# Optimization experiments

Measured on AMD Instinct MI355X. Metric: run time of the kernel, lower is better.

The kernel has to match this reference:

```python
import jax, jax.numpy as jnp
import numpy as np

C_IN = 128
C_INNER = 128


def setup_inputs() -> dict:
    key = jax.random.key(0)
    ks = jax.random.split(key, 9)
    b, c, h, w = 4, C_IN, 64, 64
    s = 1.0 / np.sqrt(c)
    x = jax.random.normal(ks[0], (b, c, h, w), dtype=jnp.float32)
    Wq = jax.random.normal(ks[1], (C_INNER, C_IN), dtype=jnp.float32) * s
    bq = jnp.zeros((C_INNER,), dtype=jnp.float32)
    Wk = jax.random.normal(ks[2], (C_INNER, C_IN), dtype=jnp.float32) * s
    bk = jnp.zeros((C_INNER,), dtype=jnp.float32)
    Wv = jax.random.normal(ks[3], (C_INNER, C_IN), dtype=jnp.float32) * s
    bv = jnp.zeros((C_INNER,), dtype=jnp.float32)
    Wo = jax.random.normal(ks[4], (C_IN, C_INNER), dtype=jnp.float32) * (1.0 / np.sqrt(C_INNER))
    bo = jnp.zeros((C_IN,), dtype=jnp.float32)
    return {"x": x, "Wq": Wq, "bq": bq, "Wk": Wk, "bk": bk,
            "Wv": Wv, "bv": bv, "Wo": Wo, "bo": bo}


def _conv1x1(x, W, bias):
    # x: (b,c,h,w), W: (o,c) -> (b,o,h,w)
    return jnp.einsum('oc,bchw->bohw', W, x) + bias[None, :, None, None]


def reference(x, Wq, bq, Wk, bk, Wv, bv, Wo, bo):
    b, c, h, w = x.shape
    ci = Wq.shape[0]
    n = h * w
    q = _conv1x1(x, Wq, bq).reshape(b, ci, n)          # (b, ci, n)
    k = _conv1x1(x, Wk, bk).reshape(b, ci, n)          # (b, ci, n)
    v = _conv1x1(x, Wv, bv).reshape(b, ci, n)          # (b, ci, n)
    # attn = softmax(q^T @ k) over keys
    attn = jnp.einsum('bci,bcj->bij', q, k)            # (b, n, n)
    attn = jax.nn.softmax(attn, axis=-1)
    out = jnp.einsum('bij,bcj->bci', attn, v)          # (b, ci, n)
    out = out.reshape(b, ci, h, w)
    out = _conv1x1(out, Wo, bo)
    return out + x
```

## Files before the change

### kernel.cpp

```cpp
#include <hip/hip_runtime.h>
#include <math.h>
#include <stdint.h>

#define CDIM 128
#define NTOT 4096

typedef _Float16 f16x8 __attribute__((ext_vector_type(8)));
typedef float floatx4 __attribute__((ext_vector_type(4)));

static __device__ __forceinline__ floatx4 mfma16(f16x8 a, f16x8 b, floatx4 c) {
    return __builtin_amdgcn_mfma_f32_16x16x32_f16(a, b, c, 0, 0, 0);
}
static __device__ __forceinline__ unsigned short f2h(float f) {
    _Float16 h = (_Float16)f;
    return __builtin_bit_cast(unsigned short, h);
}
static __device__ __forceinline__ float h2f(unsigned short u) {
    return (float)__builtin_bit_cast(_Float16, u);
}

#define SWZ(row, cc) ((((row) << 7)) + ((((cc) ^ ((row) & 15))) << 3))
#define SWZ8(row, cc) ((((row) << 6)) + ((((cc) ^ ((row) & 7))) << 3))

static __device__ __forceinline__ void gload_lds16(const void* g, void* l) {
    __builtin_amdgcn_global_load_lds(
        (const __attribute__((address_space(1))) void*)g,
        (__attribute__((address_space(3))) void*)l, 16, 0, 0);
}

__global__ __launch_bounds__(256) void wcvt_kernel(
    const float* __restrict__ Wq, const float* __restrict__ Wk,
    const float* __restrict__ Wv, const float* __restrict__ Wo,
    unsigned short* __restrict__ Wh)
{
    const float* src = (blockIdx.y == 0) ? Wq : (blockIdx.y == 1) ? Wk
                     : (blockIdx.y == 2) ? Wv : Wo;
    const int i = (blockIdx.x * 256 + threadIdx.x) * 4;
    float4 f = *(const float4*)&src[i];
    ushort4 u = { f2h(f.x), f2h(f.y), f2h(f.z), f2h(f.w) };
    *(ushort4*)&Wh[(size_t)blockIdx.y * 16384 + i] = u;
}

__global__ __launch_bounds__(256) void qkv_proj_kernel(
    const float* __restrict__ x, const unsigned short* __restrict__ Wh,
    const float* __restrict__ bq, const float* __restrict__ bk,
    const float* __restrict__ bv,
    unsigned short* __restrict__ qo, unsigned short* __restrict__ ko,
    unsigned short* __restrict__ vo)
{
    __shared__ __align__(16) unsigned short Xs[16][136];

    const int t = threadIdx.x;
    const int bid = blockIdx.x;
    const int swz = ((bid & 7) << 7) | (bid >> 3);
    const int b = swz >> 8;
    const int n0 = (swz & 255) * 16;
    const int w = t >> 6, quad = (t >> 4) & 3, l15 = t & 15;

    {
        const int n = (t & 3) * 4;
        const int c = (t >> 2) * 2;
        float4 xr[2];
        #pragma unroll
        for (int j = 0; j < 2; ++j)
            xr[j] = *(const float4*)&x[((size_t)b * CDIM + c + j) * NTOT + n0 + n];
        #pragma unroll
        for (int k = 0; k < 4; ++k) {
            ushort2 u;
            u.x = f2h(((const float*)&xr[0])[k]);
            u.y = f2h(((const float*)&xr[1])[k]);
            *(ushort2*)&Xs[n + k][c] = u;
        }
    }
    __syncthreads();

    f16x8 xf[4];
    #pragma unroll
    for (int f = 0; f < 4; ++f)
        xf[f] = *(const f16x8*)&Xs[l15][f * 32 + quad * 8];

    #pragma unroll
    for (int s = 0; s < 2; ++s) {
        const unsigned short* Wm = Wh + (size_t)s * 16384;
        const float* bias = s ? bk : bq;
        unsigned short* dst = s ? ko : qo;
        #pragma unroll
        for (int ot = 0; ot < 2; ++ot) {
            const int o = w * 32 + ot * 16;
            floatx4 acc = (floatx4){0.f, 0.f, 0.f, 0.f};
            #pragma unroll
            for (int f = 0; f < 4; ++f) {
                f16x8 aW = *(const f16x8*)
                    &Wm[(size_t)(o + l15) * CDIM + f * 32 + quad * 8];
                acc = mfma16(aW, xf[f], acc);
            }
            const int ob = o + quad * 4;
            ushort4 u;
            u.x = f2h(acc[0] + bias[ob + 0]);
            u.y = f2h(acc[1] + bias[ob + 1]);
            u.z = f2h(acc[2] + bias[ob + 2]);
            u.w = f2h(acc[3] + bias[ob + 3]);
            *(ushort4*)&dst[((size_t)b * NTOT + n0 + l15) * CDIM + ob] = u;
        }
    }
    {
        const unsigned short* Wm = Wh + 2 * 16384;
        #pragma unroll
        for (int ot = 0; ot < 2; ++ot) {
            const int o = w * 32 + ot * 16 + l15;
            floatx4 acc = (floatx4){0.f, 0.f, 0.f, 0.f};
            #pragma unroll
            for (int f = 0; f < 4; ++f) {
                f16x8 bW = *(const f16x8*)
                    &Wm[(size_t)o * CDIM + f * 32 + quad * 8];
                acc = mfma16(xf[f], bW, acc);
            }
            const float bv_ = bv[o];
            ushort4 u;
            u.x = f2h(acc[0] + bv_); u.y = f2h(acc[1] + bv_);
            u.z = f2h(acc[2] + bv_); u.w = f2h(acc[3] + bv_);
            *(ushort4*)&vo[((size_t)b * CDIM + o) * NTOT + n0 + quad * 4] = u;
        }
    }
}

__global__ __launch_bounds__(256, 2) void attn_kernel(
    const unsigned short* __restrict__ qg,
    const unsigned short* __restrict__ kg,
    const unsigned short* __restrict__ vg,
    unsigned short* __restrict__ Op,
    float* __restrict__ Ms, float* __restrict__ Ls)
{
    __shared__ __align__(16) unsigned short Kb[2][64 * 128];
    __shared__ __align__(16) unsigned short Vb[2][128 * 64];
    __shared__ __align__(16) unsigned short Ps[128 * 64];

    const int t = threadIdx.x;
    const int w = t >> 6, quad = (t >> 4) & 3, l15 = t & 15;

    const int bid = blockIdx.x;
    const int swz = ((bid & 7) << 6) | (bid >> 3);
    const int gidx = swz >> 5;
    const int b = gidx & 3;
    const int z = gidx >> 2;
    const int i0 = (swz & 31) * 128;
    const int jbase = z * 1024;
    const size_t vbase = (size_t)b * CDIM * NTOT;

    f16x8 bQ[2][4];
    #pragma unroll
    for (int nt = 0; nt < 2; ++nt) {
        const size_t qrow = ((size_t)b * NTOT + i0 + w * 32 + nt * 16 + l15) * CDIM;
        #pragma unroll
        for (int f = 0; f < 4; ++f)
            bQ[nt][f] = *(const f16x8*)&qg[qrow + f * 32 + quad * 8];
    }

    auto stage = [&](unsigned short* Kd, unsigned short* Vd, int j0) {
        const size_t kbase = ((size_t)b * NTOT + j0) * CDIM;
        const size_t vrow0 = vbase + j0;
        #pragma unroll
        for (int r = 0; r < 4; ++r) {
            const int flat = r * 256 + t;
            const int ldsoff = (r * 256 + (t & ~63)) * 8;
            const int krow = flat >> 4, kcc = flat & 15;
            gload_lds16(&kg[kbase + (size_t)krow * CDIM + ((kcc ^ (krow & 15)) << 3)],
                        &Kd[ldsoff]);
        }
        #pragma unroll
        for (int r = 0; r < 4; ++r) {
            const int flat = r * 256 + t;
            const int ldsoff = (r * 256 + (t & ~63)) * 8;
            const int vrow = flat >> 3, vcc = flat & 7;
            gload_lds16(&vg[vrow0 + (size_t)vrow * NTOT + ((vcc ^ (vrow & 7)) << 3)],
                        &Vd[ldsoff]);
        }
    };

    floatx4 accO[2][8];
    #pragma unroll
    for (int nt = 0; nt < 2; ++nt)
        #pragma unroll
        for (int dt = 0; dt < 8; ++dt) accO[nt][dt] = (floatx4){0.f, 0.f, 0.f, 0.f};
    float m_run[2] = {-INFINITY, -INFINITY};
    float l_part[2] = {0.f, 0.f};

    stage(Kb[0], Vb[0], jbase);

    for (int iter = 0; iter < 16; ++iter) {
        const int cur = iter & 1;

        asm volatile("s_waitcnt vmcnt(0) lgkmcnt(0)" ::: "memory");
        __builtin_amdgcn_s_barrier();

        if (iter < 15) stage(Kb[cur ^ 1], Vb[cur ^ 1], jbase + (iter + 1) * 64);

        floatx4 accT[2][4];
        #pragma unroll
        for (int nt = 0; nt < 2; ++nt)
            #pragma unroll
            for (int jt = 0; jt < 4; ++jt) accT[nt][jt] = (floatx4){0.f, 0.f, 0.f, 0.f};
        __builtin_amdgcn_s_setprio(1);
        #pragma unroll
        for (int jt = 0; jt < 4; ++jt)
            #pragma unroll
            for (int f = 0; f < 4; ++f) {
                f16x8 aK = *(const f16x8*)&Kb[cur][SWZ(jt * 16 + l15, f * 4 + quad)];
                accT[0][jt] = mfma16(aK, bQ[0][f], accT[0][jt]);
                accT[1][jt] = mfma16(aK, bQ[1][f], accT[1][jt]);
            }
        __builtin_amdgcn_s_setprio(0);

        ushort4 pu[2][4];
        #pragma unroll
        for (int nt = 0; nt < 2; ++nt) {
            float tm = accT[nt][0][0];
            #pragma unroll
            for (int jt = 0; jt < 4; ++jt)
                #pragma unroll
                for (int r = 0; r < 4; ++r) tm = fmaxf(tm, accT[nt][jt][r]);
            tm = fmaxf(tm, __shfl_xor(tm, 16));
            tm = fmaxf(tm, __shfl_xor(tm, 32));
            if (__ballot(tm > m_run[nt] + 8.f)) {
                const float m_new = fmaxf(m_run[nt], tm);
                const float alpha = __expf(m_run[nt] - m_new);
                m_run[nt] = m_new;
                l_part[nt] *= alpha;
                #pragma unroll
                for (int dt = 0; dt < 8; ++dt) {
                    accO[nt][dt][0] *= alpha; accO[nt][dt][1] *= alpha;
                    accO[nt][dt][2] *= alpha; accO[nt][dt][3] *= alpha;
                }
            }
            const float mcur = m_run[nt];
            float ps = 0.f;
            #pragma unroll
            for (int jt = 0; jt < 4; ++jt) {
                float p0 = __expf(accT[nt][jt][0] - mcur);
                float p1 = __expf(accT[nt][jt][1] - mcur);
                float p2 = __expf(accT[nt][jt][2] - mcur);
                float p3 = __expf(accT[nt][jt][3] - mcur);
                ps += (p0 + p1) + (p2 + p3);
                pu[nt][jt].x = f2h(p0); pu[nt][jt].y = f2h(p1);
                pu[nt][jt].z = f2h(p2); pu[nt][jt].w = f2h(p3);
            }
            l_part[nt] += ps;
        }

        #pragma unroll
        for (int nt = 0; nt < 2; ++nt) {
            const int prow = w * 32 + nt * 16 + l15;
            #pragma unroll
            for (int jt = 0; jt < 4; ++jt)
                *(ushort4*)&Ps[SWZ8(prow, 2 * jt + (quad >> 1)) + (quad & 1) * 4] =
                    pu[nt][jt];
        }
        asm volatile("s_waitcnt lgkmcnt(0)" ::: "memory");
        __builtin_amdgcn_sched_barrier(0);

        f16x8 bP[2][2];
        #pragma unroll
        for (int nt = 0; nt < 2; ++nt) {
            const int prow = w * 32 + nt * 16 + l15;
            #pragma unroll
            for (int kb = 0; kb < 2; ++kb)
                bP[nt][kb] = *(const f16x8*)&Ps[SWZ8(prow, kb * 4 + quad)];
        }
        __builtin_amdgcn_s_setprio(1);
        #pragma unroll
        for (int dt = 0; dt < 8; ++dt)
            #pragma unroll
            for (int kb = 0; kb < 2; ++kb) {
                f16x8 aV = *(const f16x8*)&Vb[cur][SWZ8(dt * 16 + l15, kb * 4 + quad)];
                accO[0][dt] = mfma16(aV, bP[0][kb], accO[0][dt]);
                accO[1][dt] = mfma16(aV, bP[1][kb], accO[1][dt]);
            }
        __builtin_amdgcn_s_setprio(0);
    }

    #pragma unroll
    for (int nt = 0; nt < 2; ++nt) {
        float lf = l_part[nt];
        lf += __shfl_xor(lf, 16);
        lf += __shfl_xor(lf, 32);
        const float inv = 1.0f / lf;
        const size_t orow =
            (((size_t)z * 4 + b) * NTOT + i0 + w * 32 + nt * 16 + l15) * CDIM;
        #pragma unroll
        for (int dt = 0; dt < 8; ++dt) {
            ushort4 u;
            u.x = f2h(accO[nt][dt][0] * inv); u.y = f2h(accO[nt][dt][1] * inv);
            u.z = f2h(accO[nt][dt][2] * inv); u.w = f2h(accO[nt][dt][3] * inv);
            *(ushort4*)&Op[orow + dt * 16 + quad * 4] = u;
        }
        if (quad == 0) {
            const int idx = (z * 4 + b) * NTOT + i0 + w * 32 + nt * 16 + l15;
            Ms[idx] = m_run[nt];
            Ls[idx] = lf;
        }
    }
}

__global__ __launch_bounds__(256) void out_proj_kernel(
    const unsigned short* __restrict__ Op,
    const float* __restrict__ Ms, const float* __restrict__ Ls,
    const unsigned short* __restrict__ Woh, const float* __restrict__ bo,
    const float* __restrict__ x, float* __restrict__ out)
{
    __shared__ __align__(16) unsigned short As[32][136];

    const int t = threadIdx.x, b = blockIdx.y, n0 = blockIdx.x * 32;
    const int zo = blockIdx.z * 64;
    const int w = t >> 6, quad = (t >> 4) & 3, l15 = t & 15;

    const size_t PER = (size_t)NTOT * 4 * CDIM;

    #pragma unroll
    for (int r = 0; r < 2; ++r) {
        int flat = r * 256 + t;
        int row = flat >> 4, c16 = (flat & 15) * 8;
        const int bn = b * NTOT + n0 + row;
        float m0 = Ms[bn], m1 = Ms[bn + 16384], m2 = Ms[bn + 32768], m3 = Ms[bn + 49152];
        float M = fmaxf(fmaxf(m0, m1), fmaxf(m2, m3));
        float w0 = Ls[bn]         * __expf(m0 - M);
        float w1 = Ls[bn + 16384] * __expf(m1 - M);
        float w2 = Ls[bn + 32768] * __expf(m2 - M);
        float w3 = Ls[bn + 49152] * __expf(m3 - M);
        const float inv = 1.0f / (w0 + w1 + w2 + w3);
        w0 *= inv; w1 *= inv; w2 *= inv; w3 *= inv;

        const size_t base = (size_t)bn * CDIM + c16;
        uint4 a0 = *(const uint4*)&Op[base];
        uint4 a1 = *(const uint4*)&Op[PER + base];
        uint4 a2 = *(const uint4*)&Op[2 * PER + base];
        uint4 a3 = *(const uint4*)&Op[3 * PER + base];
        const unsigned short* p0 = (const unsigned short*)&a0;
        const unsigned short* p1 = (const unsigned short*)&a1;
        const unsigned short* p2 = (const unsigned short*)&a2;
        const unsigned short* p3 = (const unsigned short*)&a3;
        unsigned short mv[8];
        #pragma unroll
        for (int j = 0; j < 8; ++j)
            mv[j] = f2h(w0 * h2f(p0[j]) + w1 * h2f(p1[j]) +
                        w2 * h2f(p2[j]) + w3 * h2f(p3[j]));
        *(uint4*)&As[row][c16] = *(const uint4*)mv;
    }
    __syncthreads();

    const int nt = w & 1, oh = w >> 1;
    f16x8 bA[4];
    #pragma unroll
    for (int f = 0; f < 4; ++f)
        bA[f] = *(const f16x8*)&As[nt * 16 + l15][f * 32 + quad * 8];

    #pragma unroll
    for (int ot = 0; ot < 2; ++ot) {
        const int o = zo + oh * 32 + ot * 16;
        floatx4 acc = (floatx4){0.f, 0.f, 0.f, 0.f};
        #pragma unroll
        for (int f = 0; f < 4; ++f) {
            f16x8 aW = *(const f16x8*)
                &Woh[(size_t)(o + l15) * CDIM + f * 32 + quad * 8];
            acc = mfma16(aW, bA[f], acc);
        }
        const int ob = o + quad * 4;
        #pragma unroll
        for (int r = 0; r < 4; ++r) {
            size_t idx = ((size_t)b * CDIM + ob + r) * NTOT + n0 + nt * 16 + l15;
            out[idx] = acc[r] + bo[ob + r] + x[idx];
        }
    }
}

extern "C" void kernel_launch(void* const* d_in, const int* in_sizes, int n_in,
                              void* d_out, int out_size, void* d_ws, size_t ws_size,
                              hipStream_t stream)
{
    const float* x  = (const float*)d_in[0];
    const float* Wq = (const float*)d_in[1];
    const float* bq = (const float*)d_in[2];
    const float* Wk = (const float*)d_in[3];
    const float* bk = (const float*)d_in[4];
    const float* Wv = (const float*)d_in[5];
    const float* bv = (const float*)d_in[6];
    const float* Wo = (const float*)d_in[7];
    const float* bo = (const float*)d_in[8];
    float* out = (float*)d_out;

    const size_t PER = (size_t)4 * CDIM * NTOT;
    unsigned short* q_ws  = (unsigned short*)d_ws;
    unsigned short* k_ws  = q_ws + PER;
    unsigned short* v_ws  = k_ws + PER;
    unsigned short* op_ws = v_ws + PER;
    float*          ms_ws = (float*)(op_ws + 4 * PER);
    float*          ls_ws = ms_ws + 4 * 16384;
    unsigned short* wh_ws = (unsigned short*)(ls_ws + 4 * 16384);

    wcvt_kernel<<<dim3(16, 4), dim3(256), 0, stream>>>(Wq, Wk, Wv, Wo, wh_ws);
    qkv_proj_kernel<<<dim3(1024), dim3(256), 0, stream>>>(
        x, wh_ws, bq, bk, bv, q_ws, k_ws, v_ws);
    attn_kernel<<<dim3(512), dim3(256), 0, stream>>>(
        q_ws, k_ws, v_ws, op_ws, ms_ws, ls_ws);
    out_proj_kernel<<<dim3(128, 4, 2), dim3(256), 0, stream>>>(
        op_ws, ms_ws, ls_ws, wh_ws + 3 * 16384, bo, x, out);
}
```

Before: 150.5 us.

## Shrink attention tiles to 64 queries and 32 keys with 2-wave blocks

The attention kernel now uses 128-thread blocks covering 64 query rows and walks the key range in 32-key steps over 32 iterations, doubling the grid to 1024 blocks. The K, V and P shared-memory tiles shrink and are re-indexed with a packed two-row swizzle so that 32-wide key chunks still fill 64-element LDS rows. The aim is more resident blocks per CU and better latency hiding from the smaller LDS footprint. In exchange there are more barriers per key processed, more softmax max/rescale steps per iteration, and K/V tiles are loaded by twice as many blocks, lowering reuse.

After: 160.9 us. 6.9% more time.

```diff
diff --git a/kernel.cpp b/kernel.cpp
--- a/kernel.cpp
+++ b/kernel.cpp
@@ -124,26 +124,26 @@
     }
 }
 
-__global__ __launch_bounds__(256, 2) void attn_kernel(
+__global__ __launch_bounds__(128, 2) void attn_kernel(
     const unsigned short* __restrict__ qg,
     const unsigned short* __restrict__ kg,
     const unsigned short* __restrict__ vg,
     unsigned short* __restrict__ Op,
     float* __restrict__ Ms, float* __restrict__ Ls)
 {
-    __shared__ __align__(16) unsigned short Kb[2][64 * 128];
-    __shared__ __align__(16) unsigned short Vb[2][128 * 64];
-    __shared__ __align__(16) unsigned short Ps[128 * 64];
+    __shared__ __align__(16) unsigned short Kb[2][32 * 128];
+    __shared__ __align__(16) unsigned short Vb[2][64 * 64];
+    __shared__ __align__(16) unsigned short Ps[32 * 64];
 
     const int t = threadIdx.x;
     const int w = t >> 6, quad = (t >> 4) & 3, l15 = t & 15;
 
     const int bid = blockIdx.x;
-    const int swz = ((bid & 7) << 6) | (bid >> 3);
-    const int gidx = swz >> 5;
+    const int swz = ((bid & 7) << 7) | (bid >> 3);
+    const int gidx = swz >> 6;
     const int b = gidx & 3;
     const int z = gidx >> 2;
-    const int i0 = (swz & 31) * 128;
+    const int i0 = (swz & 63) * 64;
     const int jbase = z * 1024;
     const size_t vbase = (size_t)b * CDIM * NTOT;
 
@@ -158,21 +158,22 @@
 
     auto stage = [&](unsigned short* Kd, unsigned short* Vd, int j0) {
         const size_t kbase = ((size_t)b * NTOT + j0) * CDIM;
-        const size_t vrow0 = vbase + j0;
         #pragma unroll
         for (int r = 0; r < 4; ++r) {
-            const int flat = r * 256 + t;
-            const int ldsoff = (r * 256 + (t & ~63)) * 8;
+            const int flat = r * 128 + t;
+            const int ldsoff = (r * 128 + (t & ~63)) * 8;
             const int krow = flat >> 4, kcc = flat & 15;
             gload_lds16(&kg[kbase + (size_t)krow * CDIM + ((kcc ^ (krow & 15)) << 3)],
                         &Kd[ldsoff]);
         }
         #pragma unroll
         for (int r = 0; r < 4; ++r) {
-            const int flat = r * 256 + t;
-            const int ldsoff = (r * 256 + (t & ~63)) * 8;
-            const int vrow = flat >> 3, vcc = flat & 7;
-            gload_lds16(&vg[vrow0 + (size_t)vrow * NTOT + ((vcc ^ (vrow & 7)) << 3)],
+            const int flat = r * 128 + t;
+            const int ldsoff = (r * 128 + (t & ~63)) * 8;
+            const int vrow = flat >> 3, s = flat & 7;
+            const int cc = s ^ (vrow & 7);
+            const int d = vrow * 2 + (cc >> 2), jc = cc & 3;
+            gload_lds16(&vg[vbase + (size_t)d * NTOT + j0 + jc * 8],
                         &Vd[ldsoff]);
         }
     };
@@ -187,22 +188,22 @@
 
     stage(Kb[0], Vb[0], jbase);
 
-    for (int iter = 0; iter < 16; ++iter) {
+    for (int iter = 0; iter < 32; ++iter) {
         const int cur = iter & 1;
 
         asm volatile("s_waitcnt vmcnt(0) lgkmcnt(0)" ::: "memory");
         __builtin_amdgcn_s_barrier();
 
-        if (iter < 15) stage(Kb[cur ^ 1], Vb[cur ^ 1], jbase + (iter + 1) * 64);
-
-        floatx4 accT[2][4];
+        if (iter < 31) stage(Kb[cur ^ 1], Vb[cur ^ 1], jbase + (iter + 1) * 32);
+
+        floatx4 accT[2][2];
         #pragma unroll
         for (int nt = 0; nt < 2; ++nt)
             #pragma unroll
-            for (int jt = 0; jt < 4; ++jt) accT[nt][jt] = (floatx4){0.f, 0.f, 0.f, 0.f};
+            for (int jt = 0; jt < 2; ++jt) accT[nt][jt] = (floatx4){0.f, 0.f, 0.f, 0.f};
         __builtin_amdgcn_s_setprio(1);
         #pragma unroll
-        for (int jt = 0; jt < 4; ++jt)
+        for (int jt = 0; jt < 2; ++jt)
             #pragma unroll
             for (int f = 0; f < 4; ++f) {
                 f16x8 aK = *(const f16x8*)&Kb[cur][SWZ(jt * 16 + l15, f * 4 + quad)];
@@ -211,12 +212,12 @@
             }
         __builtin_amdgcn_s_setprio(0);
 
-        ushort4 pu[2][4];
+        ushort4 pu[2][2];
         #pragma unroll
         for (int nt = 0; nt < 2; ++nt) {
             float tm = accT[nt][0][0];
             #pragma unroll
-            for (int jt = 0; jt < 4; ++jt)
+            for (int jt = 0; jt < 2; ++jt)
                 #pragma unroll
                 for (int r = 0; r < 4; ++r) tm = fmaxf(tm, accT[nt][jt][r]);
             tm = fmaxf(tm, __shfl_xor(tm, 16));
@@ -235,7 +236,7 @@
             const float mcur = m_run[nt];
             float ps = 0.f;
             #pragma unroll
-            for (int jt = 0; jt < 4; ++jt) {
+            for (int jt = 0; jt < 2; ++jt) {
                 float p0 = __expf(accT[nt][jt][0] - mcur);
                 float p1 = __expf(accT[nt][jt][1] - mcur);
                 float p2 = __expf(accT[nt][jt][2] - mcur);
@@ -249,32 +250,29 @@
 
         #pragma unroll
         for (int nt = 0; nt < 2; ++nt) {
-            const int prow = w * 32 + nt * 16 + l15;
-            #pragma unroll
-            for (int jt = 0; jt < 4; ++jt)
-                *(ushort4*)&Ps[SWZ8(prow, 2 * jt + (quad >> 1)) + (quad & 1) * 4] =
-                    pu[nt][jt];
+            const int q = w * 32 + nt * 16 + l15;
+            #pragma unroll
+            for (int jt = 0; jt < 2; ++jt)
+                *(ushort4*)&Ps[SWZ8(q >> 1, ((q & 1) << 2) + jt * 2 + (quad >> 1))
+                               + (quad & 1) * 4] = pu[nt][jt];
         }
         asm volatile("s_waitcnt lgkmcnt(0)" ::: "memory");
         __builtin_amdgcn_sched_barrier(0);
 
-        f16x8 bP[2][2];
+        f16x8 bP[2];
         #pragma unroll
         for (int nt = 0; nt < 2; ++nt) {
-            const int prow = w * 32 + nt * 16 + l15;
-            #pragma unroll
-            for (int kb = 0; kb < 2; ++kb)
-                bP[nt][kb] = *(const f16x8*)&Ps[SWZ8(prow, kb * 4 + quad)];
+            const int q = w * 32 + nt * 16 + l15;
+            bP[nt] = *(const f16x8*)&Ps[SWZ8(q >> 1, ((q & 1) << 2) + quad)];
         }
         __builtin_amdgcn_s_setprio(1);
         #pragma unroll
-        for (int dt = 0; dt < 8; ++dt)
-            #pragma unroll
-            for (int kb = 0; kb < 2; ++kb) {
-                f16x8 aV = *(const f16x8*)&Vb[cur][SWZ8(dt * 16 + l15, kb * 4 + quad)];
-                accO[0][dt] = mfma16(aV, bP[0][kb], accO[0][dt]);
-                accO[1][dt] = mfma16(aV, bP[1][kb], accO[1][dt]);
-            }
+        for (int dt = 0; dt < 8; ++dt) {
+            const int d = dt * 16 + l15;
+            f16x8 aV = *(const f16x8*)&Vb[cur][SWZ8(d >> 1, ((d & 1) << 2) + quad)];
+            accO[0][dt] = mfma16(aV, bP[0], accO[0][dt]);
+            accO[1][dt] = mfma16(aV, bP[1], accO[1][dt]);
+        }
         __builtin_amdgcn_s_setprio(0);
     }
 
@@ -399,7 +397,7 @@
     wcvt_kernel<<<dim3(16, 4), dim3(256), 0, stream>>>(Wq, Wk, Wv, Wo, wh_ws);
     qkv_proj_kernel<<<dim3(1024), dim3(256), 0, stream>>>(
         x, wh_ws, bq, bk, bv, q_ws, k_ws, v_ws);
-    attn_kernel<<<dim3(512), dim3(256), 0, stream>>>(
+    attn_kernel<<<dim3(1024), dim3(128), 0, stream>>>(
         q_ws, k_ws, v_ws, op_ws, ms_ws, ls_ws);
     out_proj_kernel<<<dim3(128, 4, 2), dim3(256), 0, stream>>>(
         op_ws, ms_ws, ls_ws, wh_ws + 3 * 16384, bo, x, out);
```

## Software-pipeline attention QK/PV stages and drop weight-conversion kernel

Applied to the files above, without the earlier changes.

The attention main loop is restructured into a skewed software pipeline. The QK^T and softmax for the current tile run alongside the PV product of the previous tile, and K and V staging are split so each buffer is refilled as soon as it is freed, with a partial vmcnt wait in place of a full drain. The separate fp32-to-fp16 weight conversion launch is removed, and the projection kernels now convert weights inline from fp32 loads. Softmax probabilities are packed with cvt_pkrtz, which rounds toward zero instead of to nearest. The cost is more complex barrier logic and twice the weight-load bandwidth in the projection kernels.

Measured after the change: 159.1 us. 5.7% more time.

```diff
diff --git a/kernel.cpp b/kernel.cpp
--- a/kernel.cpp
+++ b/kernel.cpp
@@ -17,6 +17,14 @@
 }
 static __device__ __forceinline__ float h2f(unsigned short u) {
     return (float)__builtin_bit_cast(_Float16, u);
+}
+static __device__ __forceinline__ f16x8 ldW8f(const float* p) {
+    float4 a = *(const float4*)p;
+    float4 c = *(const float4*)(p + 4);
+    f16x8 r;
+    r[0] = (_Float16)a.x; r[1] = (_Float16)a.y; r[2] = (_Float16)a.z; r[3] = (_Float16)a.w;
+    r[4] = (_Float16)c.x; r[5] = (_Float16)c.y; r[6] = (_Float16)c.z; r[7] = (_Float16)c.w;
+    return r;
 }
 
 #define SWZ(row, cc) ((((row) << 7)) + ((((cc) ^ ((row) & 15))) << 3))
@@ -28,21 +36,10 @@
         (__attribute__((address_space(3))) void*)l, 16, 0, 0);
 }
 
-__global__ __launch_bounds__(256) void wcvt_kernel(
+__global__ __launch_bounds__(256) void qkv_proj_kernel(
+    const float* __restrict__ x,
     const float* __restrict__ Wq, const float* __restrict__ Wk,
-    const float* __restrict__ Wv, const float* __restrict__ Wo,
-    unsigned short* __restrict__ Wh)
-{
-    const float* src = (blockIdx.y == 0) ? Wq : (blockIdx.y == 1) ? Wk
-                     : (blockIdx.y == 2) ? Wv : Wo;
-    const int i = (blockIdx.x * 256 + threadIdx.x) * 4;
-    float4 f = *(const float4*)&src[i];
-    ushort4 u = { f2h(f.x), f2h(f.y), f2h(f.z), f2h(f.w) };
-    *(ushort4*)&Wh[(size_t)blockIdx.y * 16384 + i] = u;
-}
-
-__global__ __launch_bounds__(256) void qkv_proj_kernel(
-    const float* __restrict__ x, const unsigned short* __restrict__ Wh,
+    const float* __restrict__ Wv,
     const float* __restrict__ bq, const float* __restrict__ bk,
     const float* __restrict__ bv,
     unsigned short* __restrict__ qo, unsigned short* __restrict__ ko,
@@ -81,7 +78,7 @@
 
     #pragma unroll
     for (int s = 0; s < 2; ++s) {
-        const unsigned short* Wm = Wh + (size_t)s * 16384;
+        const float* Wm = s ? Wk : Wq;
         const float* bias = s ? bk : bq;
         unsigned short* dst = s ? ko : qo;
         #pragma unroll
@@ -90,8 +87,7 @@
             floatx4 acc = (floatx4){0.f, 0.f, 0.f, 0.f};
             #pragma unroll
             for (int f = 0; f < 4; ++f) {
-                f16x8 aW = *(const f16x8*)
-                    &Wm[(size_t)(o + l15) * CDIM + f * 32 + quad * 8];
+                f16x8 aW = ldW8f(&Wm[(size_t)(o + l15) * CDIM + f * 32 + quad * 8]);
                 acc = mfma16(aW, xf[f], acc);
             }
             const int ob = o + quad * 4;
@@ -104,15 +100,13 @@
         }
     }
     {
-        const unsigned short* Wm = Wh + 2 * 16384;
         #pragma unroll
         for (int ot = 0; ot < 2; ++ot) {
             const int o = w * 32 + ot * 16 + l15;
             floatx4 acc = (floatx4){0.f, 0.f, 0.f, 0.f};
             #pragma unroll
             for (int f = 0; f < 4; ++f) {
-                f16x8 bW = *(const f16x8*)
-                    &Wm[(size_t)o * CDIM + f * 32 + quad * 8];
+                f16x8 bW = ldW8f(&Wv[(size_t)o * CDIM + f * 32 + quad * 8]);
                 acc = mfma16(xf[f], bW, acc);
             }
             const float bv_ = bv[o];
@@ -156,9 +150,8 @@
             bQ[nt][f] = *(const f16x8*)&qg[qrow + f * 32 + quad * 8];
     }
 
-    auto stage = [&](unsigned short* Kd, unsigned short* Vd, int j0) {
+    auto stageK = [&](unsigned short* Kd, int j0) {
         const size_t kbase = ((size_t)b * NTOT + j0) * CDIM;
-        const size_t vrow0 = vbase + j0;
         #pragma unroll
         for (int r = 0; r < 4; ++r) {
             const int flat = r * 256 + t;
@@ -167,6 +160,9 @@
             gload_lds16(&kg[kbase + (size_t)krow * CDIM + ((kcc ^ (krow & 15)) << 3)],
                         &Kd[ldsoff]);
         }
+    };
+    auto stageV = [&](unsigned short* Vd, int j0) {
+        const size_t vrow0 = vbase + j0;
         #pragma unroll
         for (int r = 0; r < 4; ++r) {
             const int flat = r * 256 + t;
@@ -185,17 +181,11 @@
     float m_run[2] = {-INFINITY, -INFINITY};
     float l_part[2] = {0.f, 0.f};
 
-    stage(Kb[0], Vb[0], jbase);
-
-    for (int iter = 0; iter < 16; ++iter) {
-        const int cur = iter & 1;
-
-        asm volatile("s_waitcnt vmcnt(0) lgkmcnt(0)" ::: "memory");
-        __builtin_amdgcn_s_barrier();
-
-        if (iter < 15) stage(Kb[cur ^ 1], Vb[cur ^ 1], jbase + (iter + 1) * 64);
-
-        floatx4 accT[2][4];
+    floatx4 accT[2][4];
+    uint2 pu[2][4];
+    f16x8 bP[2][2];
+
+    auto QK = [&](const unsigned short* Kd) {
         #pragma unroll
         for (int nt = 0; nt < 2; ++nt)
             #pragma unroll
@@ -205,13 +195,34 @@
         for (int jt = 0; jt < 4; ++jt)
             #pragma unroll
             for (int f = 0; f < 4; ++f) {
-                f16x8 aK = *(const f16x8*)&Kb[cur][SWZ(jt * 16 + l15, f * 4 + quad)];
+                f16x8 aK = *(const f16x8*)&Kd[SWZ(jt * 16 + l15, f * 4 + quad)];
                 accT[0][jt] = mfma16(aK, bQ[0][f], accT[0][jt]);
                 accT[1][jt] = mfma16(aK, bQ[1][f], accT[1][jt]);
             }
         __builtin_amdgcn_s_setprio(0);
-
-        ushort4 pu[2][4];
+    };
+    auto RB = [&]() {
+        #pragma unroll
+        for (int nt = 0; nt < 2; ++nt) {
+            const int prow = w * 32 + nt * 16 + l15;
+            #pragma unroll
+            for (int kb = 0; kb < 2; ++kb)
+                bP[nt][kb] = *(const f16x8*)&Ps[SWZ8(prow, kb * 4 + quad)];
+        }
+    };
+    auto PV = [&](const unsigned short* Vd) {
+        __builtin_amdgcn_s_setprio(1);
+        #pragma unroll
+        for (int dt = 0; dt < 8; ++dt)
+            #pragma unroll
+            for (int kb = 0; kb < 2; ++kb) {
+                f16x8 aV = *(const f16x8*)&Vd[SWZ8(dt * 16 + l15, kb * 4 + quad)];
+                accO[0][dt] = mfma16(aV, bP[0][kb], accO[0][dt]);
+                accO[1][dt] = mfma16(aV, bP[1][kb], accO[1][dt]);
+            }
+        __builtin_amdgcn_s_setprio(0);
+    };
+    auto SM = [&]() {
         #pragma unroll
         for (int nt = 0; nt < 2; ++nt) {
             float tm = accT[nt][0][0];
@@ -241,42 +252,64 @@
                 float p2 = __expf(accT[nt][jt][2] - mcur);
                 float p3 = __expf(accT[nt][jt][3] - mcur);
                 ps += (p0 + p1) + (p2 + p3);
-                pu[nt][jt].x = f2h(p0); pu[nt][jt].y = f2h(p1);
-                pu[nt][jt].z = f2h(p2); pu[nt][jt].w = f2h(p3);
+                pu[nt][jt].x = __builtin_bit_cast(unsigned int,
+                                   __builtin_amdgcn_cvt_pkrtz(p0, p1));
+                pu[nt][jt].y = __builtin_bit_cast(unsigned int,
+                                   __builtin_amdgcn_cvt_pkrtz(p2, p3));
             }
             l_part[nt] += ps;
         }
-
+    };
+    auto WP = [&]() {
         #pragma unroll
         for (int nt = 0; nt < 2; ++nt) {
             const int prow = w * 32 + nt * 16 + l15;
             #pragma unroll
             for (int jt = 0; jt < 4; ++jt)
-                *(ushort4*)&Ps[SWZ8(prow, 2 * jt + (quad >> 1)) + (quad & 1) * 4] =
+                *(uint2*)&Ps[SWZ8(prow, 2 * jt + (quad >> 1)) + (quad & 1) * 4] =
                     pu[nt][jt];
         }
+    };
+
+    stageK(Kb[0], jbase);
+    stageV(Vb[0], jbase);
+    unsigned short *Kc = Kb[0], *Kn = Kb[1], *Vc = Vb[0], *Vn = Vb[1];
+
+    asm volatile("s_waitcnt vmcnt(0) lgkmcnt(0)" ::: "memory");
+    __builtin_amdgcn_s_barrier();
+    stageK(Kn, jbase + 64);
+    stageV(Vn, jbase + 64);
+    QK(Kc);
+    SM();
+    WP();
+    { unsigned short* tp = Kc; Kc = Kn; Kn = tp; tp = Vc; Vc = Vn; Vn = tp; }
+
+    for (int it = 1; it <= 14; ++it) {
+        asm volatile("s_waitcnt vmcnt(4) lgkmcnt(0)" ::: "memory");
+        __builtin_amdgcn_s_barrier();
+        RB();
+        stageK(Kn, jbase + (it + 1) * 64);
+        QK(Kc);
+        PV(Vn);
+        SM();
         asm volatile("s_waitcnt lgkmcnt(0)" ::: "memory");
-        __builtin_amdgcn_sched_barrier(0);
-
-        f16x8 bP[2][2];
-        #pragma unroll
-        for (int nt = 0; nt < 2; ++nt) {
-            const int prow = w * 32 + nt * 16 + l15;
-            #pragma unroll
-            for (int kb = 0; kb < 2; ++kb)
-                bP[nt][kb] = *(const f16x8*)&Ps[SWZ8(prow, kb * 4 + quad)];
-        }
-        __builtin_amdgcn_s_setprio(1);
-        #pragma unroll
-        for (int dt = 0; dt < 8; ++dt)
-            #pragma unroll
-            for (int kb = 0; kb < 2; ++kb) {
-                f16x8 aV = *(const f16x8*)&Vb[cur][SWZ8(dt * 16 + l15, kb * 4 + quad)];
-                accO[0][dt] = mfma16(aV, bP[0][kb], accO[0][dt]);
-                accO[1][dt] = mfma16(aV, bP[1][kb], accO[1][dt]);
-            }
-        __builtin_amdgcn_s_setprio(0);
-    }
+        __builtin_amdgcn_s_barrier();
+        stageV(Vn, jbase + (it + 1) * 64);
+        WP();
+        { unsigned short* tp = Kc; Kc = Kn; Kn = tp; tp = Vc; Vc = Vn; Vn = tp; }
+    }
+
+    asm volatile("s_waitcnt vmcnt(4) lgkmcnt(0)" ::: "memory");
+    __builtin_amdgcn_s_barrier();
+    RB();
+    QK(Kc);
+    PV(Vn);
+    SM();
+    WP();
+    asm volatile("s_waitcnt vmcnt(0)" ::: "memory");
+    __builtin_amdgcn_s_barrier();
+    RB();
+    PV(Vc);
 
     #pragma unroll
     for (int nt = 0; nt < 2; ++nt) {
@@ -304,7 +337,7 @@
 __global__ __launch_bounds__(256) void out_proj_kernel(
     const unsigned short* __restrict__ Op,
     const float* __restrict__ Ms, const float* __restrict__ Ls,
-    const unsigned short* __restrict__ Woh, const float* __restrict__ bo,
+    const float* __restrict__ Wo, const float* __restrict__ bo,
     const float* __restrict__ x, float* __restrict__ out)
 {
     __shared__ __align__(16) unsigned short As[32][136];
@@ -359,8 +392,7 @@
         floatx4 acc = (floatx4){0.f, 0.f, 0.f, 0.f};
         #pragma unroll
         for (int f = 0; f < 4; ++f) {
-            f16x8 aW = *(const f16x8*)
-                &Woh[(size_t)(o + l15) * CDIM + f * 32 + quad * 8];
+            f16x8 aW = ldW8f(&Wo[(size_t)(o + l15) * CDIM + f * 32 + quad * 8]);
             acc = mfma16(aW, bA[f], acc);
         }
         const int ob = o + quad * 4;
@@ -394,13 +426,11 @@
     unsigned short* op_ws = v_ws + PER;
     float*          ms_ws = (float*)(op_ws + 4 * PER);
     float*          ls_ws = ms_ws + 4 * 16384;
-    unsigned short* wh_ws = (unsigned short*)(ls_ws + 4 * 16384);
-
-    wcvt_kernel<<<dim3(16, 4), dim3(256), 0, stream>>>(Wq, Wk, Wv, Wo, wh_ws);
+
     qkv_proj_kernel<<<dim3(1024), dim3(256), 0, stream>>>(
-        x, wh_ws, bq, bk, bv, q_ws, k_ws, v_ws);
+        x, Wq, Wk, Wv, bq, bk, bv, q_ws, k_ws, v_ws);
     attn_kernel<<<dim3(512), dim3(256), 0, stream>>>(
         q_ws, k_ws, v_ws, op_ws, ms_ws, ls_ws);
     out_proj_kernel<<<dim3(128, 4, 2), dim3(256), 0, stream>>>(
-        op_ws, ms_ws, ls_ws, wh_ws + 3 * 16384, bo, x, out);
-}
+        op_ws, ms_ws, ls_ws, Wo, bo, x, out);
+}
```
